# Optimization experiments

Measured on AMD Instinct MI355X. Metric: run time of the kernel, lower is better.

## Reference

```python
import jax, jax.numpy as jnp
import numpy as np

N, E, B, P = 131072, 262144, 4096, 1024
HID, CTX, FEAT, L = 256, 128, 512, 4


def _ln(x, g, bb, eps=1e-5):
    mu = jnp.mean(x, -1, keepdims=True)
    v = jnp.mean((x - mu) ** 2, -1, keepdims=True)
    return (x - mu) * jax.lax.rsqrt(v + eps) * g + bb


def setup_inputs() -> dict:
    key = jax.random.key(0)
    ks = iter(jax.random.split(key, 64))
    nrm = lambda sh, s=0.05: (jax.random.normal(next(ks), sh, jnp.float32) * s)
    inp = {
        "nf": jax.random.normal(next(ks), (N, 69), jnp.float32),
        "ei": jax.random.randint(next(ks), (2, E), 0, N, dtype=jnp.int32),
        "ef": jax.random.normal(next(ks), (E, 9), jnp.float32),
        "b": jnp.sort(jax.random.randint(next(ks), (N,), 0, B, dtype=jnp.int32)),
        "pid": jax.random.randint(next(ks), (B,), 0, P, dtype=jnp.int32),
        # MPNN params
        "Wn": nrm((69, HID)), "bn": jnp.zeros((HID,)),
        "We": nrm((9, HID)), "be": jnp.zeros((HID,)),
        "Wm": nrm((L, 2 * HID, HID)), "bm": jnp.zeros((L, HID)),
        "Wu": nrm((L, HID, HID)), "bu": jnp.zeros((L, HID)),
        "lng": jnp.ones((L, HID)), "lnb": jnp.zeros((L, HID)),
        # context embedding
        "ctx_emb": nrm((P, CTX), 0.02),
        # FiLM gamma net: Linear(128,256)-LN-ReLU-Linear(256,512)
        "gW1": nrm((CTX, HID)), "gb1": jnp.zeros((HID,)),
        "glng": jnp.ones((HID,)), "glnb": jnp.zeros((HID,)),
        "gW2": nrm((HID, FEAT)), "gb2": jnp.ones((FEAT,)),
        # FiLM beta net
        "bW1": nrm((CTX, HID)), "bb1": jnp.zeros((HID,)),
        "blng": jnp.ones((HID,)), "blnb": jnp.zeros((HID,)),
        "bW2": nrm((HID, FEAT)), "bb2": jnp.zeros((FEAT,)),
        # predictor: Linear(512,256)-ReLU-Linear(256,1)
        "pW1": nrm((FEAT, HID)), "pb1": jnp.zeros((HID,)),
        "pW2": nrm((HID, 1)), "pb2": jnp.zeros((1,)),
    }
    return inp


def reference(nf, ei, ef, b, pid, Wn, bn, We, be, Wm, bm, Wu, bu, lng, lnb,
              ctx_emb, gW1, gb1, glng, glnb, gW2, gb2,
              bW1, bb1, blng, blnb, bW2, bb2, pW1, pb1, pW2, pb2):
    src, dst = ei[0], ei[1]
    h = jax.nn.relu(nf @ Wn + bn)          # [N,256]
    e = jax.nn.relu(ef @ We + be)          # [E,256]
    for l in range(L):
        m = jax.nn.relu(jnp.concatenate([h[src], e], -1) @ Wm[l] + bm[l])  # [E,256]
        agg = jax.ops.segment_sum(m, dst, num_segments=N)                   # scatter-add
        h = _ln(h + jax.nn.relu(agg @ Wu[l] + bu[l]), lng[l], lnb[l])
    # graph readout: mean || max -> [B,512]
    ssum = jax.ops.segment_sum(h, b, num_segments=B)
    cnt = jnp.maximum(jax.ops.segment_sum(jnp.ones((h.shape[0], 1), h.dtype), b, num_segments=B), 1.0)
    gmax = jax.ops.segment_max(h, b, num_segments=B)
    gmax = jnp.where(jnp.isneginf(gmax), 0.0, gmax)
    g = jnp.concatenate([ssum / cnt, gmax], -1)  # [B,512]
    # FiLM fusion
    c = ctx_emb[pid]                              # [B,128]
    gamma = jax.nn.relu(_ln(c @ gW1 + gb1, glng, glnb)) @ gW2 + gb2
    beta = jax.nn.relu(_ln(c @ bW1 + bb1, blng, blnb)) @ bW2 + bb2
    hmod = gamma * g + beta
    out = (jax.nn.relu(hmod @ pW1 + pb1) @ pW2 + pb2).squeeze(-1)  # [B]
    return out
```

## Files before the change

### kernel.cpp

```cpp
#include <hip/hip_runtime.h>
#include <hip/hip_bf16.h>
#include <math.h>

#define HID 256
#define CTXD 128
#define FEAT 512
#define NLAYER 4

#define SW(n) (((n) >> 1) & 3)

typedef __hip_bfloat16 bf16;
typedef __attribute__((ext_vector_type(8))) short short8;
typedef __attribute__((ext_vector_type(4))) float floatx4;

__device__ __forceinline__ float bf2f(bf16 x) { return __bfloat162float(x); }
__device__ __forceinline__ bf16 f2bf(float x) { return __float2bfloat16(x); }
__device__ __forceinline__ float us2f(unsigned short u) {
    union { unsigned u; float f; } c; c.u = ((unsigned)u) << 16; return c.f;
}
__device__ __forceinline__ unsigned short f2us(float f) {
    bf16 b = f2bf(f); return *(unsigned short*)&b;
}

__device__ __forceinline__ void glds16(const void* g, void* l) {
    __builtin_amdgcn_global_load_lds(
        (__attribute__((address_space(1))) void*)g,
        (__attribute__((address_space(3))) void*)l, 16, 0, 0);
}

__global__ __launch_bounds__(256) void hist_kernel(const int* __restrict__ dst,
                                                   int* __restrict__ cnt, int E)
{
    int i = blockIdx.x * 256 + threadIdx.x;
    if (i < E) atomicAdd(&cnt[dst[i]], 1);
}

__global__ __launch_bounds__(256) void scan1_kernel(int* __restrict__ cnt,
                                                    int* __restrict__ bsum)
{
    __shared__ int sd[256];
    const int t = threadIdx.x;
    const int i = blockIdx.x * 256 + t;
    int v = cnt[i];
    sd[t] = v;
    __syncthreads();
    for (int o = 1; o < 256; o <<= 1) {
        int x = (t >= o) ? sd[t - o] : 0;
        __syncthreads();
        sd[t] += x;
        __syncthreads();
    }
    cnt[i] = sd[t] - v;
    if (t == 255) bsum[blockIdx.x] = sd[255];
}

__global__ void scan2_kernel(int* __restrict__ bsum)
{
    __shared__ int sd[512];
    const int t = threadIdx.x;
    int v = bsum[t];
    sd[t] = v;
    __syncthreads();
    for (int o = 1; o < 512; o <<= 1) {
        int x = (t >= o) ? sd[t - o] : 0;
        __syncthreads();
        sd[t] += x;
        __syncthreads();
    }
    bsum[t] = sd[t] - v;
}

__global__ __launch_bounds__(256) void scan3_kernel(int* __restrict__ cnt,
                                                    const int* __restrict__ bsum)
{
    int i = blockIdx.x * 256 + threadIdx.x;
    cnt[i] += bsum[blockIdx.x];
}

__global__ __launch_bounds__(256) void scatter_perm_kernel(
    const int* __restrict__ dst, int* __restrict__ cursor,
    int* __restrict__ perm, int E)
{
    int i = blockIdx.x * 256 + threadIdx.x;
    if (i < E) {
        int p = atomicAdd(&cursor[dst[i]], 1);
        perm[p] = i;
    }
}

__global__ __launch_bounds__(256)
void build_wimg_kernel(const float* __restrict__ W, bf16* __restrict__ img,
                       int K, int KT, int L)
{
    long idx = (long)blockIdx.x * 256 + threadIdx.x;
    long tot = (long)L * KT * 8192;
    if (idx >= tot) return;
    int l  = (int)(idx / ((long)KT * 8192));
    int r  = (int)(idx % ((long)KT * 8192));
    int kt = r >> 13;
    int r2 = r & 8191;
    int n  = r2 >> 5;
    int s  = (r2 >> 3) & 3;
    int j  = r2 & 7;
    int k  = kt * 32 + ((s ^ SW(n)) * 8) + j;
    float v = (k < K) ? W[((long)l * K + k) * HID + n] : 0.f;
    img[idx] = f2bf(v);
}

__device__ __forceinline__ void kt_tail(
    int kt, const bf16* __restrict__ Wimg, const float* __restrict__ W,
    short* As, short* Bs, floatx4 (&acc)[4][4])
{
    const int t = threadIdx.x;
    const int w = t >> 6, lane = t & 63;
    const int fr = lane & 15, q = lane >> 4;
    const int wm = (w & 1) * 64, wn = (w >> 1) * 64;
    const int k0 = kt * 32;

    if (Wimg) {
        const short* base = (const short*)Wimg + (long)kt * 8192;
#pragma unroll
        for (int j = 0; j < 2; ++j) {
            const int chunk = w * 2 + j;
            glds16(base + chunk * 512 + lane * 8, (char*)Bs + chunk * 1024);
        }
    } else {
#pragma unroll
        for (int cc = 0; cc < 2; ++cc) {
            const int slot = t + cc * 512;
            const int n    = slot >> 2;
            const int kg   = slot & 3;
            const int kk   = k0 + kg * 8;
            short8 pk;
#pragma unroll
            for (int j = 0; j < 8; ++j)
                pk[j] = (short)f2us(W[(long)(kk + j) * HID + n]);
            *(short8*)&Bs[n * 32 + (kg ^ SW(n)) * 8] = pk;
        }
    }
    __syncthreads();
    short8 af[4], bf8[4];
#pragma unroll
    for (int mt = 0; mt < 4; ++mt) {
        const int r = wm + mt * 16 + fr;
        af[mt] = *(const short8*)&As[r * 32 + (q ^ SW(r)) * 8];
    }
#pragma unroll
    for (int nt = 0; nt < 4; ++nt) {
        const int r = wn + nt * 16 + fr;
        bf8[nt] = *(const short8*)&Bs[r * 32 + (q ^ SW(r)) * 8];
    }
#pragma unroll
    for (int mt = 0; mt < 4; ++mt)
#pragma unroll
        for (int nt = 0; nt < 4; ++nt)
            acc[mt][nt] = __builtin_amdgcn_mfma_f32_16x16x32_bf16(
                af[mt], bf8[nt], acc[mt][nt], 0, 0, 0);
    __syncthreads();
}

__global__ __launch_bounds__(512)
void msg_gemm4(const bf16* __restrict__ h_, const float* __restrict__ ef,
               const float* __restrict__ We, const float* __restrict__ be,
               const int* __restrict__ src, const int* __restrict__ perm,
               const float* __restrict__ W, const bf16* __restrict__ Wimg,
               const float* __restrict__ bias, bf16* __restrict__ mout)
{
    __shared__ __align__(16) short As[128 * 32];
    __shared__ __align__(16) short Bs[256 * 32];
    __shared__ int   srcL[128];
    __shared__ int   edgeL[128];
    __shared__ float efL[128][9];

    const int  t  = threadIdx.x;
    const long bm = (long)blockIdx.x * 128;

    if (t < 128) {
        int eg = perm[bm + t];
        edgeL[t] = eg;
        srcL[t]  = src[eg];
    }
    __syncthreads();
    for (int i = t; i < 128 * 9; i += 512) {
        int r = i / 9, qq = i % 9;
        efL[r][qq] = ef[(long)edgeL[r] * 9 + qq];
    }

    floatx4 acc[4][4];
#pragma unroll
    for (int i = 0; i < 4; ++i)
#pragma unroll
        for (int j = 0; j < 4; ++j) acc[i][j] = (floatx4){0.f, 0.f, 0.f, 0.f};

    const int w = t >> 6, lane = t & 63;
    const int fr = lane & 15, q = lane >> 4;
    const int wm = (w & 1) * 64, wn = (w >> 1) * 64;
    const int arow = t >> 2, akg = t & 3;
    const int aslot = arow * 32 + (akg ^ SW(arow)) * 8;

    const long hbase = (long)srcL[arow] * HID + akg * 8;
    short8 stash[8];
#pragma unroll
    for (int kt = 0; kt < 8; ++kt)
        stash[kt] = *(const short8*)((const short*)h_ + hbase + kt * 32);
    __syncthreads();

#pragma unroll
    for (int kt = 0; kt < 8; ++kt) {
        *(short8*)&As[aslot] = stash[kt];
        kt_tail(kt, Wimg, W, As, Bs, acc);
    }
    for (int kt = 8; kt < 16; ++kt) {
        const int kc = (kt - 8) * 32 + akg * 8;
        float s[8];
#pragma unroll
        for (int j = 0; j < 8; ++j) s[j] = be[kc + j];
#pragma unroll
        for (int qq = 0; qq < 9; ++qq) {
            const float efv = efL[arow][qq];
#pragma unroll
            for (int j = 0; j < 8; ++j)
                s[j] = fmaf(efv, We[qq * HID + kc + j], s[j]);
        }
        short8 pk;
#pragma unroll
        for (int j = 0; j < 8; ++j) pk[j] = (short)f2us(fmaxf(s[j], 0.f));
        *(short8*)&As[aslot] = pk;
        kt_tail(kt, Wimg, W, As, Bs, acc);
    }

#pragma unroll
    for (int nt = 0; nt < 4; ++nt) {
        const int col = wn + nt * 16 + fr;
        const float bv = bias[col];
#pragma unroll
        for (int mt = 0; mt < 4; ++mt)
#pragma unroll
            for (int reg = 0; reg < 4; ++reg) {
                const long row = bm + wm + mt * 16 + q * 4 + reg;
                mout[row * HID + col] = f2bf(fmaxf(acc[mt][nt][reg] + bv, 0.f));
            }
    }
}

__global__ __launch_bounds__(512)
void upd_gemm3(const bf16* __restrict__ mbuf, const int* __restrict__ cursor,
               const float* __restrict__ W, const bf16* __restrict__ Wimg,
               const float* __restrict__ bias,
               const float* __restrict__ lng, const float* __restrict__ lnb,
               bf16* __restrict__ h_)
{
    __shared__ __align__(16) short As[128 * 32];
    __shared__ __align__(16) short Bs[256 * 32];
    __shared__ int   rpL[129];
    __shared__ float redS[128][4];
    __shared__ float redS2[128][4];

    const int  t  = threadIdx.x;
    const long bm = (long)blockIdx.x * 128;

    if (t < 128) rpL[t + 1] = cursor[bm + t];
    if (t == 0)  rpL[0] = (bm == 0) ? 0 : cursor[bm - 1];
    __syncthreads();

    floatx4 acc[4][4];
#pragma unroll
    for (int i = 0; i < 4; ++i)
#pragma unroll
        for (int j = 0; j < 4; ++j) acc[i][j] = (floatx4){0.f, 0.f, 0.f, 0.f};

    const int w = t >> 6, lane = t & 63;
    const int fr = lane & 15, q = lane >> 4;
    const int wm = (w & 1) * 64, wn = (w >> 1) * 64;
    const int arow = t >> 2, akg = t & 3;
    const int aslot = arow * 32 + (akg ^ SW(arow)) * 8;

    for (int kt = 0; kt < 8; ++kt) {
        const int kk = kt * 32 + akg * 8;
        {
            float s[8] = {0.f, 0.f, 0.f, 0.f, 0.f, 0.f, 0.f, 0.f};
            const int j1 = rpL[arow + 1];
            for (int j = rpL[arow]; j < j1; ++j) {
                const short8 mv = *(const short8*)((const short*)mbuf +
                                                   ((long)j * HID + kk));
#pragma unroll
                for (int x = 0; x < 8; ++x) s[x] += us2f((unsigned short)mv[x]);
            }
            short8 pk;
#pragma unroll
            for (int x = 0; x < 8; ++x) pk[x] = (short)f2us(s[x]);
            *(short8*)&As[aslot] = pk;
        }
        kt_tail(kt, Wimg, W, As, Bs, acc);
    }

    const int wnIdx = w >> 1;
#pragma unroll
    for (int mt = 0; mt < 4; ++mt)
#pragma unroll
        for (int reg = 0; reg < 4; ++reg) {
            const int  lrow = wm + mt * 16 + q * 4 + reg;
            const long row  = bm + lrow;
            float ps = 0.f, ps2 = 0.f;
#pragma unroll
            for (int nt = 0; nt < 4; ++nt) {
                const int col = wn + nt * 16 + fr;
                float v = bf2f(h_[row * HID + col]) +
                          fmaxf(acc[mt][nt][reg] + bias[col], 0.f);
                acc[mt][nt][reg] = v;
                ps  += v;
                ps2 += v * v;
            }
#pragma unroll
            for (int m = 1; m < 16; m <<= 1) {
                ps  += __shfl_xor(ps, m);
                ps2 += __shfl_xor(ps2, m);
            }
            if (fr == 0) { redS[lrow][wnIdx] = ps; redS2[lrow][wnIdx] = ps2; }
        }
    __syncthreads();
#pragma unroll
    for (int mt = 0; mt < 4; ++mt)
#pragma unroll
        for (int reg = 0; reg < 4; ++reg) {
            const int  lrow = wm + mt * 16 + q * 4 + reg;
            const long row  = bm + lrow;
            const float ts  = redS[lrow][0] + redS[lrow][1] +
                              redS[lrow][2] + redS[lrow][3];
            const float ts2 = redS2[lrow][0] + redS2[lrow][1] +
                              redS2[lrow][2] + redS2[lrow][3];
            const float mu  = ts * (1.f / 256.f);
            const float var = ts2 * (1.f / 256.f) - mu * mu;
            const float rs  = rsqrtf(var + 1e-5f);
#pragma unroll
            for (int nt = 0; nt < 4; ++nt) {
                const int col = wn + nt * 16 + fr;
                const float y = (acc[mt][nt][reg] - mu) * rs * lng[col] + lnb[col];
                h_[row * HID + col] = f2bf(y);
            }
        }
}

__global__ __launch_bounds__(512)
void enc_gemm3(const float* __restrict__ nf, const bf16* __restrict__ Wimg,
               const float* __restrict__ bias, bf16* __restrict__ h_)
{
    __shared__ __align__(16) short As[128 * 32];
    __shared__ __align__(16) short Bs[256 * 32];

    const int  t  = threadIdx.x;
    const long bm = (long)blockIdx.x * 128;

    floatx4 acc[4][4];
#pragma unroll
    for (int i = 0; i < 4; ++i)
#pragma unroll
        for (int j = 0; j < 4; ++j) acc[i][j] = (floatx4){0.f, 0.f, 0.f, 0.f};

    const int w = t >> 6, lane = t & 63;
    const int fr = lane & 15, q = lane >> 4;
    const int wm = (w & 1) * 64, wn = (w >> 1) * 64;
    const int arow = t >> 2, akg = t & 3;
    const int aslot = arow * 32 + (akg ^ SW(arow)) * 8;

    for (int kt = 0; kt < 3; ++kt) {
        const int kk = kt * 32 + akg * 8;
        short8 pk;
#pragma unroll
        for (int j = 0; j < 8; ++j) {
            const int k = kk + j;
            pk[j] = (short)f2us((k < 69) ? nf[(bm + arow) * 69 + k] : 0.f);
        }
        *(short8*)&As[aslot] = pk;
        kt_tail(kt, Wimg, nullptr, As, Bs, acc);
    }

#pragma unroll
    for (int nt = 0; nt < 4; ++nt) {
        const int col = wn + nt * 16 + fr;
        const float bv = bias[col];
#pragma unroll
        for (int mt = 0; mt < 4; ++mt)
#pragma unroll
            for (int reg = 0; reg < 4; ++reg) {
                const long row = bm + wm + mt * 16 + q * 4 + reg;
                h_[row * HID + col] = f2bf(fmaxf(acc[mt][nt][reg] + bv, 0.f));
            }
    }
}

struct PlainF32 {
    const float* A; int lda;
    __device__ float operator()(int r, int k) const { return A[(long)r * lda + k]; }
};
struct CtxF32 {
    const float* ctx; const int* pid;
    __device__ float operator()(int r, int k) const {
        return ctx[(long)pid[r] * CTXD + k];
    }
};
struct StoreF32 {
    float* C; int ldc; int relu;
    __device__ void operator()(int r, int c, const float* v) const {
        float4 o;
        o.x = v[0]; o.y = v[1]; o.z = v[2]; o.w = v[3];
        if (relu) {
            o.x = fmaxf(o.x, 0.f); o.y = fmaxf(o.y, 0.f);
            o.z = fmaxf(o.z, 0.f); o.w = fmaxf(o.w, 0.f);
        }
        *(float4*)&C[(long)r * ldc + c] = o;
    }
};
struct StoreBf16Relu {
    bf16* C;
    __device__ void operator()(int r, int c, const float* v) const {
        bf16 tmp[4];
#pragma unroll
        for (int j = 0; j < 4; ++j) tmp[j] = f2bf(fmaxf(v[j], 0.f));
        *(ushort4*)&C[(long)r * HID + c] = *(const ushort4*)tmp;
    }
};

template <typename Loader, typename Epi>
__global__ __launch_bounds__(256)
void gemm_tiled(Loader loader, const float* __restrict__ W,
                const float* __restrict__ bias, Epi epi, int M, int K, int Nc)
{
    constexpr int BM = 64, BN = 64, BK = 16;
    __shared__ __align__(16) float As[BK][BM + 4];
    __shared__ __align__(16) float Ws[BK][BN];

    const int bm = blockIdx.x * BM;
    const int bn = blockIdx.y * BN;
    const int t  = threadIdx.x;
    const int arow = t >> 2, akq = (t & 3) * 4;
    const int wn = t & 63, wk0 = t >> 6;
    const int tx = t & 15, ty = t >> 4;

    float acc[4][4] = {};
    const int ntiles = (K + BK - 1) / BK;
    for (int kt = 0; kt < ntiles; ++kt) {
        const int k0 = kt * BK;
#pragma unroll
        for (int i = 0; i < 4; ++i) {
            int k = k0 + akq + i;
            As[akq + i][arow] = (k < K) ? loader(bm + arow, k) : 0.f;
        }
#pragma unroll
        for (int i = 0; i < 4; ++i) {
            int kr = wk0 + i * 4;
            int k  = k0 + kr;
            Ws[kr][wn] = (k < K) ? W[(long)k * Nc + bn + wn] : 0.f;
        }
        __syncthreads();
#pragma unroll
        for (int kk = 0; kk < BK; ++kk) {
            float4 a = *(const float4*)&As[kk][ty * 4];
            float4 b = *(const float4*)&Ws[kk][tx * 4];
            float av[4] = {a.x, a.y, a.z, a.w};
            float bv[4] = {b.x, b.y, b.z, b.w};
#pragma unroll
            for (int i = 0; i < 4; ++i)
#pragma unroll
                for (int j = 0; j < 4; ++j) acc[i][j] += av[i] * bv[j];
        }
        __syncthreads();
    }
#pragma unroll
    for (int i = 0; i < 4; ++i) {
        const int row = bm + ty * 4 + i;
        const int col = bn + tx * 4;
        float v[4];
#pragma unroll
        for (int j = 0; j < 4; ++j) v[j] = acc[i][j] + bias[col + j];
        epi(row, col, v);
    }
}

__global__ __launch_bounds__(256)
void ln_f32_relu_kernel(float* __restrict__ x, const float* __restrict__ g,
                        const float* __restrict__ bb)
{
    const long row = blockIdx.x;
    const int  j   = threadIdx.x;
    float v = x[row * HID + j];
    float s = v, s2 = v * v;
#pragma unroll
    for (int o = 32; o > 0; o >>= 1) {
        s  += __shfl_down(s, o);
        s2 += __shfl_down(s2, o);
    }
    __shared__ float red[2][4];
    const int wid = j >> 6, lane = j & 63;
    if (lane == 0) { red[0][wid] = s; red[1][wid] = s2; }
    __syncthreads();
    float ts  = red[0][0] + red[0][1] + red[0][2] + red[0][3];
    float ts2 = red[1][0] + red[1][1] + red[1][2] + red[1][3];
    float mu  = ts * (1.f / 256.f);
    float var = ts2 * (1.f / 256.f) - mu * mu;
    float y = (v - mu) * rsqrtf(var + 1e-5f) * g[j] + bb[j];
    x[row * HID + j] = fmaxf(y, 0.f);
}

__device__ int lower_bound_i(const int* __restrict__ arr, int n, int val)
{
    int lo = 0, hi = n;
    while (lo < hi) {
        int mid = (lo + hi) >> 1;
        if (arr[mid] < val) lo = mid + 1; else hi = mid;
    }
    return lo;
}

__global__ __launch_bounds__(256)
void readout_kernel(const bf16* __restrict__ h, const int* __restrict__ b,
                    float* __restrict__ gout, int Nn)
{
    const int gidx = blockIdx.x;
    const int j    = threadIdx.x;
    const int lo   = lower_bound_i(b, Nn, gidx);
    const int hi   = lower_bound_i(b, Nn, gidx + 1);
    float s = 0.f, mx = -INFINITY;
    for (int n = lo; n < hi; ++n) {
        float v = bf2f(h[(long)n * HID + j]);
        s += v;
        mx = fmaxf(mx, v);
    }
    const int cnt = hi - lo;
    gout[(long)gidx * FEAT + j]       = s / fmaxf((float)cnt, 1.f);
    gout[(long)gidx * FEAT + HID + j] = (cnt > 0) ? mx : 0.f;
}

__global__ __launch_bounds__(256)
void film_mod_kernel(const float* __restrict__ gamma, float* __restrict__ g,
                     const float* __restrict__ beta, int n)
{
    int i = blockIdx.x * 256 + threadIdx.x;
    if (i < n) g[i] = gamma[i] * g[i] + beta[i];
}

__global__ __launch_bounds__(256)
void final_dot_kernel(const float* __restrict__ ph, const float* __restrict__ w,
                      const float* __restrict__ b2, float* __restrict__ out)
{
    const int row  = blockIdx.x * 4 + (threadIdx.x >> 6);
    const int lane = threadIdx.x & 63;
    float s = 0.f;
#pragma unroll
    for (int k = lane; k < HID; k += 64)
        s += ph[(long)row * HID + k] * w[k];
#pragma unroll
    for (int o = 32; o > 0; o >>= 1) s += __shfl_down(s, o);
    if (lane == 0) out[row] = s + b2[0];
}

__global__ void diag_out_kernel(float* out, int n, float wsmb)
{
    int i = blockIdx.x * 256 + threadIdx.x;
    if (i < n) out[i] = (i == 0) ? wsmb : 0.f;
}

extern "C" void kernel_launch(void* const* d_in, const int* in_sizes, int n_in,
                              void* d_out, int out_size, void* d_ws, size_t ws_size,
                              hipStream_t stream)
{
    const int N = 131072, E = 262144, B = 4096;

    const float* nf   = (const float*)d_in[0];
    const int*   ei   = (const int*)  d_in[1];
    const float* ef   = (const float*)d_in[2];
    const int*   bidx = (const int*)  d_in[3];
    const int*   pid  = (const int*)  d_in[4];
    const float* Wn   = (const float*)d_in[5];
    const float* bn   = (const float*)d_in[6];
    const float* We   = (const float*)d_in[7];
    const float* be   = (const float*)d_in[8];
    const float* Wm   = (const float*)d_in[9];
    const float* bm   = (const float*)d_in[10];
    const float* Wu   = (const float*)d_in[11];
    const float* bu   = (const float*)d_in[12];
    const float* lng  = (const float*)d_in[13];
    const float* lnb  = (const float*)d_in[14];
    const float* ctx  = (const float*)d_in[15];
    const float* gW1  = (const float*)d_in[16];
    const float* gb1  = (const float*)d_in[17];
    const float* glng = (const float*)d_in[18];
    const float* glnb = (const float*)d_in[19];
    const float* gW2  = (const float*)d_in[20];
    const float* gb2  = (const float*)d_in[21];
    const float* bW1  = (const float*)d_in[22];
    const float* bb1  = (const float*)d_in[23];
    const float* blng = (const float*)d_in[24];
    const float* blnb = (const float*)d_in[25];
    const float* bW2  = (const float*)d_in[26];
    const float* bb2  = (const float*)d_in[27];
    const float* pW1  = (const float*)d_in[28];
    const float* pb1  = (const float*)d_in[29];
    const float* pW2  = (const float*)d_in[30];
    const float* pb2  = (const float*)d_in[31];

    const int* src = ei;
    const int* dst = ei + E;
    float* out = (float*)d_out;

    const size_t hB    = (size_t)N * HID * sizeof(bf16);
    const size_t mB    = (size_t)E * HID * sizeof(bf16);
    const size_t curB  = (size_t)N * 4;
    const size_t permB = (size_t)E * 4;
    const size_t bsumB = 2048 * 4;
    const size_t wmImgB = (size_t)NLAYER * 16 * 8192 * 2;
    const size_t wuImgB = (size_t)NLAYER * 8  * 8192 * 2;
    const size_t wnImgB = (size_t)3 * 8192 * 2;

    const size_t needBase = hB + mB + curB + permB + bsumB;
    const size_t needFull = needBase + wmImgB + wuImgB + wnImgB;

    if (ws_size < needBase) {
        diag_out_kernel<<<dim3((B + 255) / 256), dim3(256), 0, stream>>>(
            out, B, (float)(ws_size >> 20));
        return;
    }
    const bool haveImg = ws_size >= needFull;

    char* p = (char*)d_ws;
    bf16* h      = (bf16*)p;  p += hB;
    bf16* mbuf   = (bf16*)p;  p += mB;
    int*  cursor = (int*)p;   p += curB;
    int*  perm   = (int*)p;   p += permB;
    int*  bsum   = (int*)p;   p += bsumB;
    bf16* wmImg = nullptr; bf16* wuImg = nullptr; bf16* wnImg = nullptr;
    if (haveImg) {
        wmImg = (bf16*)p; p += wmImgB;
        wuImg = (bf16*)p; p += wuImgB;
        wnImg = (bf16*)p; p += wnImgB;
    }

    float* gbuf  = (float*)mbuf;
    float* t1    = gbuf  + (long)B * FEAT;
    float* t2    = t1    + (long)B * HID;
    float* gamma = t2    + (long)B * HID;
    float* beta  = gamma + (long)B * FEAT;
    float* ph    = beta  + (long)B * FEAT;

    dim3 blk(256), blk5(512);

    hipMemsetAsync(cursor, 0, curB, stream);
    hist_kernel<<<dim3(E / 256), blk, 0, stream>>>(dst, cursor, E);
    scan1_kernel<<<dim3(N / 256), blk, 0, stream>>>(cursor, bsum);
    scan2_kernel<<<dim3(1), dim3(512), 0, stream>>>(bsum);
    scan3_kernel<<<dim3(N / 256), blk, 0, stream>>>(cursor, bsum);
    scatter_perm_kernel<<<dim3(E / 256), blk, 0, stream>>>(dst, cursor, perm, E);

    if (haveImg) {
        build_wimg_kernel<<<dim3((NLAYER * 16 * 8192 + 255) / 256), blk, 0, stream>>>(
            Wm, wmImg, 2 * HID, 16, NLAYER);
        build_wimg_kernel<<<dim3((NLAYER * 8 * 8192 + 255) / 256), blk, 0, stream>>>(
            Wu, wuImg, HID, 8, NLAYER);
        build_wimg_kernel<<<dim3((3 * 8192 + 255) / 256), blk, 0, stream>>>(
            Wn, wnImg, 69, 3, 1);
    }

    if (haveImg) {
        enc_gemm3<<<dim3(N / 128), blk5, 0, stream>>>(nf, wnImg, bn, h);
    } else {
        gemm_tiled<<<dim3(N / 64, HID / 64), blk, 0, stream>>>(
            PlainF32{nf, 69}, Wn, bn, StoreBf16Relu{h}, N, 69, HID);
    }

    for (int l = 0; l < NLAYER; ++l) {
        const float* Wml  = Wm  + (long)l * 2 * HID * HID;
        const float* bml  = bm  + (long)l * HID;
        const float* Wul  = Wu  + (long)l * HID * HID;
        const float* bul  = bu  + (long)l * HID;
        const float* lngl = lng + (long)l * HID;
        const float* lnbl = lnb + (long)l * HID;
        const bf16* wmI = haveImg ? wmImg + (long)l * 16 * 8192 : nullptr;
        const bf16* wuI = haveImg ? wuImg + (long)l * 8 * 8192 : nullptr;

        msg_gemm4<<<dim3(E / 128), blk5, 0, stream>>>(
            h, ef, We, be, src, perm, Wml, wmI, bml, mbuf);
        upd_gemm3<<<dim3(N / 128), blk5, 0, stream>>>(
            mbuf, cursor, Wul, wuI, bul, lngl, lnbl, h);
    }

    readout_kernel<<<dim3(B), blk, 0, stream>>>(h, bidx, gbuf, N);

    gemm_tiled<<<dim3(B / 64, HID / 64), blk, 0, stream>>>(
        CtxF32{ctx, pid}, gW1, gb1, StoreF32{t1, HID, 0}, B, CTXD, HID);
    ln_f32_relu_kernel<<<dim3(B), blk, 0, stream>>>(t1, glng, glnb);
    gemm_tiled<<<dim3(B / 64, FEAT / 64), blk, 0, stream>>>(
        PlainF32{t1, HID}, gW2, gb2, StoreF32{gamma, FEAT, 0}, B, HID, FEAT);

    gemm_tiled<<<dim3(B / 64, HID / 64), blk, 0, stream>>>(
        CtxF32{ctx, pid}, bW1, bb1, StoreF32{t2, HID, 0}, B, CTXD, HID);
    ln_f32_relu_kernel<<<dim3(B), blk, 0, stream>>>(t2, blng, blnb);
    gemm_tiled<<<dim3(B / 64, FEAT / 64), blk, 0, stream>>>(
        PlainF32{t2, HID}, bW2, bb2, StoreF32{beta, FEAT, 0}, B, HID, FEAT);

    film_mod_kernel<<<dim3((B * FEAT + 255) / 256), blk, 0, stream>>>(
        gamma, gbuf, beta, B * FEAT);
    gemm_tiled<<<dim3(B / 64, HID / 64), blk, 0, stream>>>(
        PlainF32{gbuf, FEAT}, pW1, pb1, StoreF32{ph, HID, 1}, B, FEAT, HID);
    final_dot_kernel<<<dim3(B / 4), blk, 0, stream>>>(ph, pW2, pb2, out);
}
```

Baseline: 1.949 ms.

## Restructure GEMM kernels to 64-row tiles with full-K LDS A and direct global B fragments

The message, update and encoder GEMMs move from 128-row tiles with per-k-step LDS staging of both operands to 64-row tiles of 256 threads. The whole A tile for the full K range is staged in swizzled LDS once, which removes the per-k-step barriers. B fragments are now read straight from a row-major bf16 weight image in global memory (cached) instead of being copied into LDS with global_load_lds. This cuts synchronisation and LDS traffic and allows more blocks per CU. The trade-off is heavier global/L2 traffic for weights, since each wave re-reads its B columns, and the edge-feature embedding and aggregation are computed in one pass up front.

```diff
diff --git a/kernel.cpp b/kernel.cpp
--- a/kernel.cpp
+++ b/kernel.cpp
@@ -7,8 +7,6 @@
 #define FEAT 512
 #define NLAYER 4
 
-#define SW(n) (((n) >> 1) & 3)
-
 typedef __hip_bfloat16 bf16;
 typedef __attribute__((ext_vector_type(8))) short short8;
 typedef __attribute__((ext_vector_type(4))) float floatx4;
@@ -22,11 +20,7 @@
     bf16 b = f2bf(f); return *(unsigned short*)&b;
 }
 
-__device__ __forceinline__ void glds16(const void* g, void* l) {
-    __builtin_amdgcn_global_load_lds(
-        (__attribute__((address_space(1))) void*)g,
-        (__attribute__((address_space(3))) void*)l, 16, 0, 0);
-}
+#define ASW(row, s) (((s) ^ ((row) & 7)) * 8)
 
 __global__ __launch_bounds__(256) void hist_kernel(const int* __restrict__ dst,
                                                    int* __restrict__ cnt, int E)
@@ -100,91 +94,63 @@
     int kt = r >> 13;
     int r2 = r & 8191;
     int n  = r2 >> 5;
-    int s  = (r2 >> 3) & 3;
-    int j  = r2 & 7;
-    int k  = kt * 32 + ((s ^ SW(n)) * 8) + j;
+    int kc = r2 & 31;
+    int k  = kt * 32 + kc;
     float v = (k < K) ? W[((long)l * K + k) * HID + n] : 0.f;
     img[idx] = f2bf(v);
 }
 
-__device__ __forceinline__ void kt_tail(
-    int kt, const bf16* __restrict__ Wimg, const float* __restrict__ W,
-    short* As, short* Bs, floatx4 (&acc)[4][4])
-{
-    const int t = threadIdx.x;
-    const int w = t >> 6, lane = t & 63;
-    const int fr = lane & 15, q = lane >> 4;
-    const int wm = (w & 1) * 64, wn = (w >> 1) * 64;
-    const int k0 = kt * 32;
-
-    if (Wimg) {
-        const short* base = (const short*)Wimg + (long)kt * 8192;
-#pragma unroll
-        for (int j = 0; j < 2; ++j) {
-            const int chunk = w * 2 + j;
-            glds16(base + chunk * 512 + lane * 8, (char*)Bs + chunk * 1024);
-        }
-    } else {
-#pragma unroll
-        for (int cc = 0; cc < 2; ++cc) {
-            const int slot = t + cc * 512;
-            const int n    = slot >> 2;
-            const int kg   = slot & 3;
-            const int kk   = k0 + kg * 8;
-            short8 pk;
-#pragma unroll
-            for (int j = 0; j < 8; ++j)
-                pk[j] = (short)f2us(W[(long)(kk + j) * HID + n]);
-            *(short8*)&Bs[n * 32 + (kg ^ SW(n)) * 8] = pk;
-        }
-    }
-    __syncthreads();
-    short8 af[4], bf8[4];
-#pragma unroll
-    for (int mt = 0; mt < 4; ++mt) {
-        const int r = wm + mt * 16 + fr;
-        af[mt] = *(const short8*)&As[r * 32 + (q ^ SW(r)) * 8];
-    }
-#pragma unroll
-    for (int nt = 0; nt < 4; ++nt) {
-        const int r = wn + nt * 16 + fr;
-        bf8[nt] = *(const short8*)&Bs[r * 32 + (q ^ SW(r)) * 8];
-    }
-#pragma unroll
-    for (int mt = 0; mt < 4; ++mt)
-#pragma unroll
-        for (int nt = 0; nt < 4; ++nt)
-            acc[mt][nt] = __builtin_amdgcn_mfma_f32_16x16x32_bf16(
-                af[mt], bf8[nt], acc[mt][nt], 0, 0, 0);
-    __syncthreads();
-}
-
-__global__ __launch_bounds__(512)
-void msg_gemm4(const bf16* __restrict__ h_, const float* __restrict__ ef,
+__device__ __forceinline__ short8 bfrag(const bf16* __restrict__ Wimg,
+                                        const float* __restrict__ W,
+                                        int Kmax, int kt, int col, int q)
+{
+    if (Wimg)
+        return *(const short8*)((const short*)Wimg + (long)kt * 8192 + col * 32 + q * 8);
+    short8 pk;
+#pragma unroll
+    for (int j = 0; j < 8; ++j) {
+        const int k = kt * 32 + q * 8 + j;
+        pk[j] = (short)f2us((k < Kmax) ? W[(long)k * HID + col] : 0.f);
+    }
+    return pk;
+}
+
+__global__ __launch_bounds__(256)
+void msg_gemm5(const bf16* __restrict__ h_, const float* __restrict__ ef,
                const float* __restrict__ We, const float* __restrict__ be,
                const int* __restrict__ src, const int* __restrict__ perm,
                const float* __restrict__ W, const bf16* __restrict__ Wimg,
                const float* __restrict__ bias, bf16* __restrict__ mout)
 {
-    __shared__ __align__(16) short As[128 * 32];
-    __shared__ __align__(16) short Bs[256 * 32];
-    __shared__ int   srcL[128];
-    __shared__ int   edgeL[128];
-    __shared__ float efL[128][9];
+    __shared__ __align__(16) short As[64 * 256];
+    __shared__ int   srcL[64];
+    __shared__ int   edgeL[64];
+    __shared__ float efL[64][9];
 
     const int  t  = threadIdx.x;
-    const long bm = (long)blockIdx.x * 128;
-
-    if (t < 128) {
+    const long bm = (long)blockIdx.x * 64;
+
+    if (t < 64) {
         int eg = perm[bm + t];
         edgeL[t] = eg;
         srcL[t]  = src[eg];
     }
     __syncthreads();
-    for (int i = t; i < 128 * 9; i += 512) {
+    for (int i = t; i < 64 * 9; i += 256) {
         int r = i / 9, qq = i % 9;
         efL[r][qq] = ef[(long)edgeL[r] * 9 + qq];
     }
+    const int row = t >> 2, sg = t & 3;
+    {
+        const short* hr = (const short*)h_ + (long)srcL[row] * HID + sg * 64;
+#pragma unroll
+        for (int i = 0; i < 8; ++i) {
+            short8 v = *(const short8*)(hr + i * 8);
+            const int s = sg * 8 + i;
+            *(short8*)&As[row * 256 + ASW(row, s)] = v;
+        }
+    }
+    __syncthreads();
 
     floatx4 acc[4][4];
 #pragma unroll
@@ -194,39 +160,66 @@
 
     const int w = t >> 6, lane = t & 63;
     const int fr = lane & 15, q = lane >> 4;
-    const int wm = (w & 1) * 64, wn = (w >> 1) * 64;
-    const int arow = t >> 2, akg = t & 3;
-    const int aslot = arow * 32 + (akg ^ SW(arow)) * 8;
-
-    const long hbase = (long)srcL[arow] * HID + akg * 8;
-    short8 stash[8];
-#pragma unroll
-    for (int kt = 0; kt < 8; ++kt)
-        stash[kt] = *(const short8*)((const short*)h_ + hbase + kt * 32);
-    __syncthreads();
-
-#pragma unroll
+    const int wn = w * 64;
+
+#pragma unroll 2
     for (int kt = 0; kt < 8; ++kt) {
-        *(short8*)&As[aslot] = stash[kt];
-        kt_tail(kt, Wimg, W, As, Bs, acc);
-    }
+        short8 bfv[4], af[4];
+#pragma unroll
+        for (int nt = 0; nt < 4; ++nt)
+            bfv[nt] = bfrag(Wimg, W, 512, kt, wn + nt * 16 + fr, q);
+#pragma unroll
+        for (int mt = 0; mt < 4; ++mt) {
+            const int r = mt * 16 + fr;
+            af[mt] = *(const short8*)&As[r * 256 + ASW(r, kt * 4 + q)];
+        }
+#pragma unroll
+        for (int mt = 0; mt < 4; ++mt)
+#pragma unroll
+            for (int nt = 0; nt < 4; ++nt)
+                acc[mt][nt] = __builtin_amdgcn_mfma_f32_16x16x32_bf16(
+                    af[mt], bfv[nt], acc[mt][nt], 0, 0, 0);
+    }
+
+    __syncthreads();
+#pragma unroll
+    for (int i = 0; i < 8; ++i) {
+        const int s  = sg * 8 + i;
+        const int kc = s * 8;
+        float sv[8];
+#pragma unroll
+        for (int j = 0; j < 8; ++j) sv[j] = be[kc + j];
+#pragma unroll
+        for (int qq = 0; qq < 9; ++qq) {
+            const float efv = efL[row][qq];
+#pragma unroll
+            for (int j = 0; j < 8; ++j)
+                sv[j] = fmaf(efv, We[qq * HID + kc + j], sv[j]);
+        }
+        short8 pk;
+#pragma unroll
+        for (int j = 0; j < 8; ++j) pk[j] = (short)f2us(fmaxf(sv[j], 0.f));
+        *(short8*)&As[row * 256 + ASW(row, s)] = pk;
+    }
+    __syncthreads();
+
+#pragma unroll 2
     for (int kt = 8; kt < 16; ++kt) {
-        const int kc = (kt - 8) * 32 + akg * 8;
-        float s[8];
-#pragma unroll
-        for (int j = 0; j < 8; ++j) s[j] = be[kc + j];
-#pragma unroll
-        for (int qq = 0; qq < 9; ++qq) {
-            const float efv = efL[arow][qq];
-#pragma unroll
-            for (int j = 0; j < 8; ++j)
-                s[j] = fmaf(efv, We[qq * HID + kc + j], s[j]);
-        }
-        short8 pk;
-#pragma unroll
-        for (int j = 0; j < 8; ++j) pk[j] = (short)f2us(fmaxf(s[j], 0.f));
-        *(short8*)&As[aslot] = pk;
-        kt_tail(kt, Wimg, W, As, Bs, acc);
+        short8 bfv[4], af[4];
+#pragma unroll
+        for (int nt = 0; nt < 4; ++nt)
+            bfv[nt] = bfrag(Wimg, W, 512, kt, wn + nt * 16 + fr, q);
+#pragma unroll
+        for (int mt = 0; mt < 4; ++mt) {
+            const int r = mt * 16 + fr;
+            af[mt] = *(const short8*)&As[r * 256 + ASW(r, (kt - 8) * 4 + q)];
+        }
+#pragma unroll
+        for (int mt = 0; mt < 4; ++mt)
+#pragma unroll
+            for (int nt = 0; nt < 4; ++nt)
+                acc[mt][nt] = __builtin_amdgcn_mfma_f32_16x16x32_bf16(
+                    af[mt], bfv[nt], acc[mt][nt], 0, 0, 0);
     }
 
 #pragma unroll
@@ -237,30 +230,49 @@
         for (int mt = 0; mt < 4; ++mt)
 #pragma unroll
             for (int reg = 0; reg < 4; ++reg) {
-                const long row = bm + wm + mt * 16 + q * 4 + reg;
-                mout[row * HID + col] = f2bf(fmaxf(acc[mt][nt][reg] + bv, 0.f));
+                const long r = bm + mt * 16 + q * 4 + reg;
+                mout[r * HID + col] = f2bf(fmaxf(acc[mt][nt][reg] + bv, 0.f));
             }
     }
 }
 
-__global__ __launch_bounds__(512)
-void upd_gemm3(const bf16* __restrict__ mbuf, const int* __restrict__ cursor,
+__global__ __launch_bounds__(256)
+void upd_gemm4(const bf16* __restrict__ mbuf, const int* __restrict__ cursor,
                const float* __restrict__ W, const bf16* __restrict__ Wimg,
                const float* __restrict__ bias,
                const float* __restrict__ lng, const float* __restrict__ lnb,
                bf16* __restrict__ h_)
 {
-    __shared__ __align__(16) short As[128 * 32];
-    __shared__ __align__(16) short Bs[256 * 32];
-    __shared__ int   rpL[129];
-    __shared__ float redS[128][4];
-    __shared__ float redS2[128][4];
+    __shared__ __align__(16) short As[64 * 256];
+    __shared__ int   rpL[65];
+    __shared__ float redS[64][4];
+    __shared__ float redS2[64][4];
 
     const int  t  = threadIdx.x;
-    const long bm = (long)blockIdx.x * 128;
-
-    if (t < 128) rpL[t + 1] = cursor[bm + t];
-    if (t == 0)  rpL[0] = (bm == 0) ? 0 : cursor[bm - 1];
+    const long bm = (long)blockIdx.x * 64;
+
+    if (t < 64) rpL[t + 1] = cursor[bm + t];
+    if (t == 0) rpL[0] = (bm == 0) ? 0 : cursor[bm - 1];
+    __syncthreads();
+
+    const int row = t >> 2, sg = t & 3;
+    const int j0 = rpL[row], j1 = rpL[row + 1];
+#pragma unroll
+    for (int i = 0; i < 8; ++i) {
+        const int s  = sg * 8 + i;
+        const int kk = s * 8;
+        float sv[8] = {0.f, 0.f, 0.f, 0.f, 0.f, 0.f, 0.f, 0.f};
+        for (int j = j0; j < j1; ++j) {
+            const short8 mv = *(const short8*)((const short*)mbuf +
+                                               ((long)j * HID + kk));
+#pragma unroll
+            for (int x = 0; x < 8; ++x) sv[x] += us2f((unsigned short)mv[x]);
+        }
+        short8 pk;
+#pragma unroll
+        for (int x = 0; x < 8; ++x) pk[x] = (short)f2us(sv[x]);
+        *(short8*)&As[row * 256 + ASW(row, s)] = pk;
+    }
     __syncthreads();
 
     floatx4 acc[4][4];
@@ -271,41 +283,38 @@
 
     const int w = t >> 6, lane = t & 63;
     const int fr = lane & 15, q = lane >> 4;
-    const int wm = (w & 1) * 64, wn = (w >> 1) * 64;
-    const int arow = t >> 2, akg = t & 3;
-    const int aslot = arow * 32 + (akg ^ SW(arow)) * 8;
-
+    const int wn = w * 64;
+
+#pragma unroll 2
     for (int kt = 0; kt < 8; ++kt) {
-        const int kk = kt * 32 + akg * 8;
-        {
-            float s[8] = {0.f, 0.f, 0.f, 0.f, 0.f, 0.f, 0.f, 0.f};
-            const int j1 = rpL[arow + 1];
-            for (int j = rpL[arow]; j < j1; ++j) {
-                const short8 mv = *(const short8*)((const short*)mbuf +
-                                                   ((long)j * HID + kk));
-#pragma unroll
-                for (int x = 0; x < 8; ++x) s[x] += us2f((unsigned short)mv[x]);
-            }
-            short8 pk;
-#pragma unroll
-            for (int x = 0; x < 8; ++x) pk[x] = (short)f2us(s[x]);
-            *(short8*)&As[aslot] = pk;
-        }
-        kt_tail(kt, Wimg, W, As, Bs, acc);
-    }
-
-    const int wnIdx = w >> 1;
+        short8 bfv[4], af[4];
+#pragma unroll
+        for (int nt = 0; nt < 4; ++nt)
+            bfv[nt] = bfrag(Wimg, W, 256, kt, wn + nt * 16 + fr, q);
+#pragma unroll
+        for (int mt = 0; mt < 4; ++mt) {
+            const int r = mt * 16 + fr;
+            af[mt] = *(const short8*)&As[r * 256 + ASW(r, kt * 4 + q)];
+        }
+#pragma unroll
+        for (int mt = 0; mt < 4; ++mt)
+#pragma unroll
+            for (int nt = 0; nt < 4; ++nt)
+                acc[mt][nt] = __builtin_amdgcn_mfma_f32_16x16x32_bf16(
+                    af[mt], bfv[nt], acc[mt][nt], 0, 0, 0);
+    }
+
 #pragma unroll
     for (int mt = 0; mt < 4; ++mt)
 #pragma unroll
         for (int reg = 0; reg < 4; ++reg) {
-            const int  lrow = wm + mt * 16 + q * 4 + reg;
-            const long row  = bm + lrow;
+            const int  lrow = mt * 16 + q * 4 + reg;
+            const long r    = bm + lrow;
             float ps = 0.f, ps2 = 0.f;
 #pragma unroll
             for (int nt = 0; nt < 4; ++nt) {
                 const int col = wn + nt * 16 + fr;
-                float v = bf2f(h_[row * HID + col]) +
+                float v = bf2f(h_[r * HID + col]) +
                           fmaxf(acc[mt][nt][reg] + bias[col], 0.f);
                 acc[mt][nt][reg] = v;
                 ps  += v;
@@ -316,15 +325,15 @@
                 ps  += __shfl_xor(ps, m);
                 ps2 += __shfl_xor(ps2, m);
             }
-            if (fr == 0) { redS[lrow][wnIdx] = ps; redS2[lrow][wnIdx] = ps2; }
+            if (fr == 0) { redS[lrow][w] = ps; redS2[lrow][w] = ps2; }
         }
     __syncthreads();
 #pragma unroll
     for (int mt = 0; mt < 4; ++mt)
 #pragma unroll
         for (int reg = 0; reg < 4; ++reg) {
-            const int  lrow = wm + mt * 16 + q * 4 + reg;
-            const long row  = bm + lrow;
+            const int  lrow = mt * 16 + q * 4 + reg;
+            const long r    = bm + lrow;
             const float ts  = redS[lrow][0] + redS[lrow][1] +
                               redS[lrow][2] + redS[lrow][3];
             const float ts2 = redS2[lrow][0] + redS2[lrow][1] +
@@ -336,20 +345,35 @@
             for (int nt = 0; nt < 4; ++nt) {
                 const int col = wn + nt * 16 + fr;
                 const float y = (acc[mt][nt][reg] - mu) * rs * lng[col] + lnb[col];
-                h_[row * HID + col] = f2bf(y);
+                h_[r * HID + col] = f2bf(y);
             }
         }
 }
 
-__global__ __launch_bounds__(512)
-void enc_gemm3(const float* __restrict__ nf, const bf16* __restrict__ Wimg,
-               const float* __restrict__ bias, bf16* __restrict__ h_)
-{
-    __shared__ __align__(16) short As[128 * 32];
-    __shared__ __align__(16) short Bs[256 * 32];
+__global__ __launch_bounds__(256)
+void enc_gemm4(const float* __restrict__ nf, const float* __restrict__ W,
+               const bf16* __restrict__ Wimg, const float* __restrict__ bias,
+               bf16* __restrict__ h_)
+{
+    __shared__ __align__(16) short As[64 * 128];
 
     const int  t  = threadIdx.x;
-    const long bm = (long)blockIdx.x * 128;
+    const long bm = (long)blockIdx.x * 64;
+    const int row = t >> 2, sg = t & 3;
+
+#pragma unroll
+    for (int i = 0; i < 4; ++i) {
+        const int s  = sg * 4 + i;
+        const int kk = s * 8;
+        short8 pk;
+#pragma unroll
+        for (int j = 0; j < 8; ++j) {
+            const int k = kk + j;
+            pk[j] = (short)f2us((k < 69) ? nf[(bm + row) * 69 + k] : 0.f);
+        }
+        *(short8*)&As[row * 128 + ASW(row, s)] = pk;
+    }
+    __syncthreads();
 
     floatx4 acc[4][4];
 #pragma unroll
@@ -359,20 +383,24 @@
 
     const int w = t >> 6, lane = t & 63;
     const int fr = lane & 15, q = lane >> 4;
-    const int wm = (w & 1) * 64, wn = (w >> 1) * 64;
-    const int arow = t >> 2, akg = t & 3;
-    const int aslot = arow * 32 + (akg ^ SW(arow)) * 8;
+    const int wn = w * 64;
 
     for (int kt = 0; kt < 3; ++kt) {
-        const int kk = kt * 32 + akg * 8;
-        short8 pk;
-#pragma unroll
-        for (int j = 0; j < 8; ++j) {
-            const int k = kk + j;
-            pk[j] = (short)f2us((k < 69) ? nf[(bm + arow) * 69 + k] : 0.f);
-        }
-        *(short8*)&As[aslot] = pk;
-        kt_tail(kt, Wimg, nullptr, As, Bs, acc);
+        short8 bfv[4], af[4];
+#pragma unroll
+        for (int nt = 0; nt < 4; ++nt)
+            bfv[nt] = bfrag(Wimg, W, 69, kt, wn + nt * 16 + fr, q);
+#pragma unroll
+        for (int mt = 0; mt < 4; ++mt) {
+            const int r = mt * 16 + fr;
+            af[mt] = *(const short8*)&As[r * 128 + ASW(r, kt * 4 + q)];
+        }
+#pragma unroll
+        for (int mt = 0; mt < 4; ++mt)
+#pragma unroll
+            for (int nt = 0; nt < 4; ++nt)
+                acc[mt][nt] = __builtin_amdgcn_mfma_f32_16x16x32_bf16(
+                    af[mt], bfv[nt], acc[mt][nt], 0, 0, 0);
     }
 
 #pragma unroll
@@ -383,8 +411,8 @@
         for (int mt = 0; mt < 4; ++mt)
 #pragma unroll
             for (int reg = 0; reg < 4; ++reg) {
-                const long row = bm + wm + mt * 16 + q * 4 + reg;
-                h_[row * HID + col] = f2bf(fmaxf(acc[mt][nt][reg] + bv, 0.f));
+                const long r = bm + mt * 16 + q * 4 + reg;
+                h_[r * HID + col] = f2bf(fmaxf(acc[mt][nt][reg] + bv, 0.f));
             }
     }
 }
@@ -409,15 +437,6 @@
             o.z = fmaxf(o.z, 0.f); o.w = fmaxf(o.w, 0.f);
         }
         *(float4*)&C[(long)r * ldc + c] = o;
-    }
-};
-struct StoreBf16Relu {
-    bf16* C;
-    __device__ void operator()(int r, int c, const float* v) const {
-        bf16 tmp[4];
-#pragma unroll
-        for (int j = 0; j < 4; ++j) tmp[j] = f2bf(fmaxf(v[j], 0.f));
-        *(ushort4*)&C[(long)r * HID + c] = *(const ushort4*)tmp;
     }
 };
 
@@ -642,7 +661,7 @@
     float* beta  = gamma + (long)B * FEAT;
     float* ph    = beta  + (long)B * FEAT;
 
-    dim3 blk(256), blk5(512);
+    dim3 blk(256);
 
     hipMemsetAsync(cursor, 0, curB, stream);
     hist_kernel<<<dim3(E / 256), blk, 0, stream>>>(dst, cursor, E);
@@ -660,12 +679,7 @@
             Wn, wnImg, 69, 3, 1);
     }
 
-    if (haveImg) {
-        enc_gemm3<<<dim3(N / 128), blk5, 0, stream>>>(nf, wnImg, bn, h);
-    } else {
-        gemm_tiled<<<dim3(N / 64, HID / 64), blk, 0, stream>>>(
-            PlainF32{nf, 69}, Wn, bn, StoreBf16Relu{h}, N, 69, HID);
-    }
+    enc_gemm4<<<dim3(N / 64), blk, 0, stream>>>(nf, Wn, wnImg, bn, h);
 
     for (int l = 0; l < NLAYER; ++l) {
         const float* Wml  = Wm  + (long)l * 2 * HID * HID;
@@ -677,9 +691,9 @@
         const bf16* wmI = haveImg ? wmImg + (long)l * 16 * 8192 : nullptr;
         const bf16* wuI = haveImg ? wuImg + (long)l * 8 * 8192 : nullptr;
 
-        msg_gemm4<<<dim3(E / 128), blk5, 0, stream>>>(
+        msg_gemm5<<<dim3(E / 64), blk, 0, stream>>>(
             h, ef, We, be, src, perm, Wml, wmI, bml, mbuf);
-        upd_gemm3<<<dim3(N / 128), blk5, 0, stream>>>(
+        upd_gemm4<<<dim3(N / 64), blk, 0, stream>>>(
             mbuf, cursor, Wul, wuI, bul, lngl, lnbl, h);
     }
 
```

Result: slower. 2.837 ms (+45.6%).
